# Optimization experiments

Measured on AMD Instinct MI355X. Metric: run time of the kernel, lower is better.

## Reference

```python
import jax, jax.numpy as jnp
import numpy as np

N_T, D_MODEL, RANK, BATCH = 64, 1024, 8, 4096
THRESHOLD = 0.0  # jumprelu threshold (forward default)


def setup_inputs() -> dict:
    key = jax.random.key(0)
    k_x, k_v, k_u, k_e = jax.random.split(key, 4)
    scale = (1.0 / (D_MODEL * RANK)) ** 0.25
    x = jax.random.normal(k_x, (BATCH, D_MODEL), dtype=jnp.float32)
    V = jax.random.normal(k_v, (N_T, RANK, D_MODEL), dtype=jnp.float32) * scale
    U = jax.random.normal(k_u, (N_T, D_MODEL, RANK), dtype=jnp.float32) * scale
    encoder = jax.random.normal(k_e, (N_T, D_MODEL), dtype=jnp.float32)
    encoder = encoder / jnp.linalg.norm(encoder, axis=1, keepdims=True)
    bias = -jnp.ones((N_T,), dtype=jnp.float32)  # init_constant(bias, -1.0)
    return {"x": x, "V": V, "U": U, "encoder": encoder, "bias": bias}


def jumprelu(x, threshold=THRESHOLD):
    # forward: hard threshold x * 1[x > threshold]
    return x * (x > threshold).astype(x.dtype)


def reference(x, V, U, encoder, bias):
    # pre_acts: (batch, n)
    pre_acts = x @ encoder.T - bias
    gate = jumprelu(pre_acts)  # activation_fn='jumprelu', threshold=0.0
    # Vx: (n, batch, rank)
    Vx = jnp.einsum('nrd,bd->nbr', V, x)
    # UVx: (n, batch, d) -- the large intermediate a fused kernel would avoid
    UVx = jnp.einsum('ndr,nbr->nbd', U, Vx)
    # gated sum over transforms: (batch, d)
    output = jnp.einsum('nbd,bn->bd', UVx, gate)
    u_norms = jnp.linalg.norm(U.reshape(U.shape[0], -1), axis=1)
    v_norms = jnp.linalg.norm(V.reshape(V.shape[0], -1), axis=1)
    frobenius_norms = u_norms * v_norms / (D_MODEL * RANK) ** 0.5
    return output, gate, frobenius_norms
```

## Files before the change

### kernel.cpp

```cpp
#include <hip/hip_runtime.h>
#include <math.h>

#define BATCHN 4096
#define DMODEL 1024
#define NT 64
#define RANK 8
#define K2 512

typedef __attribute__((ext_vector_type(8))) short bf16x8;
typedef __attribute__((ext_vector_type(4))) float f32x4;

__device__ __forceinline__ short f2bf_hu(float f) {
    unsigned u = __builtin_bit_cast(unsigned, f);
    return (short)((u + 0x8000u) >> 16);
}

__device__ __forceinline__ short f2bf(float f) {
    unsigned u = __builtin_bit_cast(unsigned, f);
    u += 0x7fffu + ((u >> 16) & 1u);
    return (short)(u >> 16);
}

__device__ __forceinline__ bf16x8 cvt8(const float* __restrict__ p) {
    float4 v0 = *(const float4*)p;
    float4 v1 = *(const float4*)(p + 4);
    bf16x8 o;
    o[0] = f2bf_hu(v0.x); o[1] = f2bf_hu(v0.y); o[2] = f2bf_hu(v0.z); o[3] = f2bf_hu(v0.w);
    o[4] = f2bf_hu(v1.x); o[5] = f2bf_hu(v1.y); o[6] = f2bf_hu(v1.z); o[7] = f2bf_hu(v1.w);
    return o;
}

__global__ __launch_bounds__(256) void gatevx_norms_kernel(
    const float* __restrict__ x, const float* __restrict__ V,
    const float* __restrict__ U, const float* __restrict__ enc,
    const float* __restrict__ bias,
    float* __restrict__ gate, float* __restrict__ fro,
    unsigned short* __restrict__ vx)
{
    __shared__ unsigned short As[64 * 128];
    __shared__ unsigned short Bs[64 * 128];
    __shared__ float red[8];
    const int bid = blockIdx.x, t = threadIdx.x;
    const int wave = t >> 6, lane = t & 63;
    const int wm = wave & 1, wn = wave >> 1;
    const int l15 = lane & 15, lq = lane >> 4;

    if (bid < 576) {
        const int bn = bid % 9, bm = bid / 9;
        const float* Brow = (bn == 0) ? enc : (V + (size_t)(bn - 1) * 64 * DMODEL);
        f32x4 acc[2][2] = {};
        for (int k0 = 0; k0 < DMODEL; k0 += 128) {
            #pragma unroll
            for (int c = 0; c < 4; ++c) {
                const int row = wave * 16 + c * 4 + lq;
                const int g = l15 ^ (row & 15);
                bf16x8 oa = cvt8(x + (size_t)(bm * 64 + row) * DMODEL + k0 + g * 8);
                *(bf16x8*)&As[row * 128 + l15 * 8] = oa;
                bf16x8 ob = cvt8(Brow + (size_t)row * DMODEL + k0 + g * 8);
                *(bf16x8*)&Bs[row * 128 + l15 * 8] = ob;
            }
            __syncthreads();
            #pragma unroll
            for (int s = 0; s < 4; ++s) {
                const int kc = s * 4 + lq;
                bf16x8 af[2], bfr[2];
                #pragma unroll
                for (int i = 0; i < 2; ++i) {
                    const int m = wm * 32 + i * 16 + l15;
                    af[i] = *(const bf16x8*)&As[m * 128 + ((kc ^ (m & 15)) * 8)];
                }
                #pragma unroll
                for (int j = 0; j < 2; ++j) {
                    const int n = wn * 32 + j * 16 + l15;
                    bfr[j] = *(const bf16x8*)&Bs[n * 128 + ((kc ^ (n & 15)) * 8)];
                }
                #pragma unroll
                for (int i = 0; i < 2; ++i)
                    #pragma unroll
                    for (int j = 0; j < 2; ++j)
                        acc[i][j] = __builtin_amdgcn_mfma_f32_16x16x32_bf16(
                            af[i], bfr[j], acc[i][j], 0, 0, 0);
            }
            __syncthreads();
        }
        #pragma unroll
        for (int i = 0; i < 2; ++i) {
            const int rowb = bm * 64 + wm * 32 + i * 16 + lq * 4;
            #pragma unroll
            for (int j = 0; j < 2; ++j) {
                const int col = wn * 32 + j * 16 + l15;
                #pragma unroll
                for (int r = 0; r < 4; ++r) {
                    const int row = rowb + r;
                    const float v = acc[i][j][r];
                    if (bn == 0) {
                        const float p = v - bias[col];
                        gate[(size_t)row * NT + col] = p > 0.f ? p : 0.f;
                    } else {
                        vx[(size_t)row * K2 + (bn - 1) * 64 + col] = (unsigned short)f2bf(v);
                    }
                }
            }
        }
    } else {
        const int n = bid - 576;
        const float* Up = U + (size_t)n * (DMODEL * RANK);
        const float* Vp = V + (size_t)n * (DMODEL * RANK);
        float su = 0.f, sv = 0.f;
        for (int i = t * 4; i < DMODEL * RANK; i += 1024) {
            float4 a = *(const float4*)(Up + i);
            su += a.x * a.x + a.y * a.y + a.z * a.z + a.w * a.w;
            float4 b = *(const float4*)(Vp + i);
            sv += b.x * b.x + b.y * b.y + b.z * b.z + b.w * b.w;
        }
        #pragma unroll
        for (int off = 32; off; off >>= 1) {
            su += __shfl_down(su, off);
            sv += __shfl_down(sv, off);
        }
        if ((t & 63) == 0) { red[wave * 2] = su; red[wave * 2 + 1] = sv; }
        __syncthreads();
        if (t == 0) {
            float tu = red[0] + red[2] + red[4] + red[6];
            float tv = red[1] + red[3] + red[5] + red[7];
            fro[n] = sqrtf(tu) * sqrtf(tv) / sqrtf((float)(DMODEL * RANK));
        }
    }
}

__global__ __launch_bounds__(256) void out_kernel(
    const unsigned short* __restrict__ vx, const float* __restrict__ gate,
    const float* __restrict__ U, float* __restrict__ out)
{
    __shared__ unsigned short As[64 * 128];
    __shared__ unsigned short Bs[16 * 64 * 8];
    const int t = threadIdx.x;
    const int wave = t >> 6, lane = t & 63;
    const int bm = blockIdx.y, bn = blockIdx.x;
    const int wm = wave & 1, wn = wave >> 1;
    const int l15 = lane & 15, lq = lane >> 4;

    f32x4 acc[2][2] = {};

    for (int k0 = 0; k0 < K2; k0 += 128) {
        const int nb = k0 >> 3;
        #pragma unroll
        for (int i = 0; i < 4; ++i) {
            const int row = wave * 16 + i * 4 + lq;
            const int grow = bm * 64 + row;
            const int g = l15 ^ (row & 15);
            bf16x8 v = *(const bf16x8*)(vx + (size_t)grow * K2 + k0 + g * 8);
            const float gs = gate[(size_t)grow * NT + nb + g];
            bf16x8 o;
            #pragma unroll
            for (int e = 0; e < 8; ++e) {
                const float f = __builtin_bit_cast(float,
                    ((unsigned)(unsigned short)v[e]) << 16);
                o[e] = (short)(__builtin_bit_cast(unsigned, f * gs) >> 16);
            }
            *(bf16x8*)&As[row * 128 + l15 * 8] = o;
        }
        #pragma unroll
        for (int c = 0; c < 4; ++c) {
            const int kc = c * 4 + wave;
            bf16x8 o = cvt8(U + (size_t)(nb + kc) * (DMODEL * RANK)
                              + (size_t)(bn * 64 + lane) * RANK);
            *(bf16x8*)&Bs[kc * 512 + lane * 8] = o;
        }
        __syncthreads();
        #pragma unroll
        for (int s = 0; s < 4; ++s) {
            const int kc = s * 4 + lq;
            bf16x8 af[2], bfr[2];
            #pragma unroll
            for (int i = 0; i < 2; ++i) {
                const int m = wm * 32 + i * 16 + l15;
                af[i] = *(const bf16x8*)&As[m * 128 + ((kc ^ (m & 15)) * 8)];
            }
            #pragma unroll
            for (int j = 0; j < 2; ++j) {
                const int n = wn * 32 + j * 16 + l15;
                bfr[j] = *(const bf16x8*)&Bs[kc * 512 + n * 8];
            }
            #pragma unroll
            for (int i = 0; i < 2; ++i)
                #pragma unroll
                for (int j = 0; j < 2; ++j)
                    acc[i][j] = __builtin_amdgcn_mfma_f32_16x16x32_bf16(
                        af[i], bfr[j], acc[i][j], 0, 0, 0);
        }
        __syncthreads();
    }

    #pragma unroll
    for (int i = 0; i < 2; ++i) {
        const int rowb = bm * 64 + wm * 32 + i * 16 + lq * 4;
        #pragma unroll
        for (int j = 0; j < 2; ++j) {
            const int col = bn * 64 + wn * 32 + j * 16 + l15;
            #pragma unroll
            for (int r = 0; r < 4; ++r)
                out[(size_t)(rowb + r) * DMODEL + col] = acc[i][j][r];
        }
    }
}

extern "C" void kernel_launch(void* const* d_in, const int* in_sizes, int n_in,
                              void* d_out, int out_size, void* d_ws, size_t ws_size,
                              hipStream_t stream) {
    const float* x    = (const float*)d_in[0];
    const float* V    = (const float*)d_in[1];
    const float* U    = (const float*)d_in[2];
    const float* enc  = (const float*)d_in[3];
    const float* bias = (const float*)d_in[4];

    float* out  = (float*)d_out;
    float* gate = out + (size_t)BATCHN * DMODEL;
    float* fro  = gate + (size_t)BATCHN * NT;
    unsigned short* vx = (unsigned short*)d_ws;

    gatevx_norms_kernel<<<640, 256, 0, stream>>>(x, V, U, enc, bias, gate, fro, vx);
    out_kernel<<<dim3(16, 64), 256, 0, stream>>>(vx, gate, U, out);
}
```

Measured before the change: 121.0 us.

## Fuse both stages into one persistent kernel with grid barriers and bf16 pre-conversion

Merges the gate/Vx/norms kernel and the output kernel into a single 1024-block kernel separated by software grid barriers. A first phase converts x, encoder/V and U to bf16 in workspace, so the GEMM stages can stage tiles with direct global-to-LDS async loads instead of per-thread fp32 loads and conversions. This aims to cut one launch and reduce load/convert cost in the inner loops. In exchange it adds an extra pass over all inputs, a memset, and spin barriers that need all 1024 blocks co-resident and fall through on timeout, which is a deadlock or correctness risk.

```diff
diff --git a/kernel.cpp b/kernel.cpp
--- a/kernel.cpp
+++ b/kernel.cpp
@@ -9,6 +9,12 @@
 
 typedef __attribute__((ext_vector_type(8))) short bf16x8;
 typedef __attribute__((ext_vector_type(4))) float f32x4;
+
+__device__ __forceinline__ void async16(void* lds, const void* g) {
+    __builtin_amdgcn_global_load_lds(
+        (const __attribute__((address_space(1))) void*)g,
+        (__attribute__((address_space(3))) void*)lds, 16, 0, 0);
+}
 
 __device__ __forceinline__ short f2bf_hu(float f) {
     unsigned u = __builtin_bit_cast(unsigned, f);
@@ -30,12 +36,29 @@
     return o;
 }
 
-__global__ __launch_bounds__(256) void gatevx_norms_kernel(
+__device__ __forceinline__ void grid_barrier(unsigned* c, unsigned n) {
+    __syncthreads();
+    if (threadIdx.x == 0) {
+        __threadfence();
+        atomicAdd(c, 1u);
+        unsigned spins = 0;
+        while (__hip_atomic_load(c, __ATOMIC_RELAXED, __HIP_MEMORY_SCOPE_AGENT) < n) {
+            __builtin_amdgcn_s_sleep(2);
+            if (++spins > 1000000u) break;
+        }
+        __threadfence();
+    }
+    __syncthreads();
+}
+
+__global__ __launch_bounds__(256, 4) void fused_kernel(
     const float* __restrict__ x, const float* __restrict__ V,
     const float* __restrict__ U, const float* __restrict__ enc,
     const float* __restrict__ bias,
-    float* __restrict__ gate, float* __restrict__ fro,
-    unsigned short* __restrict__ vx)
+    float* __restrict__ out, float* __restrict__ gate, float* __restrict__ fro,
+    unsigned short* __restrict__ xb, unsigned short* __restrict__ Wb,
+    unsigned short* __restrict__ Ub, unsigned short* __restrict__ vx,
+    unsigned* __restrict__ counters)
 {
     __shared__ unsigned short As[64 * 128];
     __shared__ unsigned short Bs[64 * 128];
@@ -45,19 +68,41 @@
     const int wm = wave & 1, wn = wave >> 1;
     const int l15 = lane & 15, lq = lane >> 4;
 
+    {
+        const int tid = bid * 256 + t;
+        for (int c = tid; c < 663552; c += 262144) {
+            const float* src;
+            unsigned short* dst;
+            if (c < 524288) {
+                src = x + (size_t)c * 8; dst = xb + (size_t)c * 8;
+            } else if (c < 598016) {
+                const int e = (c - 524288) * 8;
+                const int row = e >> 10, col = e & 1023;
+                src = (row < 64) ? (enc + (size_t)row * 1024 + col)
+                                 : (V + (size_t)(row - 64) * 1024 + col);
+                dst = Wb + e;
+            } else {
+                const int e = (c - 598016) * 8;
+                src = U + e; dst = Ub + e;
+            }
+            *(bf16x8*)dst = cvt8(src);
+        }
+    }
+    grid_barrier(&counters[0], (unsigned)gridDim.x);
+
     if (bid < 576) {
         const int bn = bid % 9, bm = bid / 9;
-        const float* Brow = (bn == 0) ? enc : (V + (size_t)(bn - 1) * 64 * DMODEL);
         f32x4 acc[2][2] = {};
+        const size_t Abase = (size_t)bm * 64 * DMODEL;
+        const size_t Bbase = (size_t)bn * 64 * DMODEL;
         for (int k0 = 0; k0 < DMODEL; k0 += 128) {
             #pragma unroll
             for (int c = 0; c < 4; ++c) {
-                const int row = wave * 16 + c * 4 + lq;
+                const int r0 = wave * 16 + c * 4;
+                const int row = r0 + lq;
                 const int g = l15 ^ (row & 15);
-                bf16x8 oa = cvt8(x + (size_t)(bm * 64 + row) * DMODEL + k0 + g * 8);
-                *(bf16x8*)&As[row * 128 + l15 * 8] = oa;
-                bf16x8 ob = cvt8(Brow + (size_t)row * DMODEL + k0 + g * 8);
-                *(bf16x8*)&Bs[row * 128 + l15 * 8] = ob;
+                async16(&As[r0 * 128], xb + Abase + (size_t)row * DMODEL + k0 + g * 8);
+                async16(&Bs[r0 * 128], Wb + Bbase + (size_t)row * DMODEL + k0 + g * 8);
             }
             __syncthreads();
             #pragma unroll
@@ -102,7 +147,7 @@
                 }
             }
         }
-    } else {
+    } else if (bid < 640) {
         const int n = bid - 576;
         const float* Up = U + (size_t)n * (DMODEL * RANK);
         const float* Vp = V + (size_t)n * (DMODEL * RANK);
@@ -126,81 +171,70 @@
             fro[n] = sqrtf(tu) * sqrtf(tv) / sqrtf((float)(DMODEL * RANK));
         }
     }
-}
-
-__global__ __launch_bounds__(256) void out_kernel(
-    const unsigned short* __restrict__ vx, const float* __restrict__ gate,
-    const float* __restrict__ U, float* __restrict__ out)
-{
-    __shared__ unsigned short As[64 * 128];
-    __shared__ unsigned short Bs[16 * 64 * 8];
-    const int t = threadIdx.x;
-    const int wave = t >> 6, lane = t & 63;
-    const int bm = blockIdx.y, bn = blockIdx.x;
-    const int wm = wave & 1, wn = wave >> 1;
-    const int l15 = lane & 15, lq = lane >> 4;
-
-    f32x4 acc[2][2] = {};
-
-    for (int k0 = 0; k0 < K2; k0 += 128) {
-        const int nb = k0 >> 3;
+    grid_barrier(&counters[1], (unsigned)gridDim.x);
+
+    {
+        const int bn = bid & 15, bm = bid >> 4;
+        f32x4 acc[2][2] = {};
+        for (int k0 = 0; k0 < K2; k0 += 128) {
+            const int nb = k0 >> 3;
+            #pragma unroll
+            for (int i = 0; i < 4; ++i) {
+                const int row = wave * 16 + i * 4 + lq;
+                const int grow = bm * 64 + row;
+                const int g = l15 ^ (row & 15);
+                bf16x8 v = *(const bf16x8*)(vx + (size_t)grow * K2 + k0 + g * 8);
+                const float gs = gate[(size_t)grow * NT + nb + g];
+                bf16x8 o;
+                #pragma unroll
+                for (int e = 0; e < 8; ++e) {
+                    const float f = __builtin_bit_cast(float,
+                        ((unsigned)(unsigned short)v[e]) << 16);
+                    o[e] = (short)(__builtin_bit_cast(unsigned, f * gs) >> 16);
+                }
+                *(bf16x8*)&As[row * 128 + l15 * 8] = o;
+            }
+            #pragma unroll
+            for (int c = 0; c < 4; ++c) {
+                const int kc = c * 4 + wave;
+                async16(&Bs[kc * 512],
+                        Ub + (size_t)(nb + kc) * (DMODEL * RANK)
+                           + (size_t)(bn * 64 + lane) * RANK);
+            }
+            __syncthreads();
+            #pragma unroll
+            for (int s = 0; s < 4; ++s) {
+                const int kc = s * 4 + lq;
+                bf16x8 af[2], bfr[2];
+                #pragma unroll
+                for (int i = 0; i < 2; ++i) {
+                    const int m = wm * 32 + i * 16 + l15;
+                    af[i] = *(const bf16x8*)&As[m * 128 + ((kc ^ (m & 15)) * 8)];
+                }
+                #pragma unroll
+                for (int j = 0; j < 2; ++j) {
+                    const int n = wn * 32 + j * 16 + l15;
+                    bfr[j] = *(const bf16x8*)&Bs[kc * 512 + n * 8];
+                }
+                #pragma unroll
+                for (int i = 0; i < 2; ++i)
+                    #pragma unroll
+                    for (int j = 0; j < 2; ++j)
+                        acc[i][j] = __builtin_amdgcn_mfma_f32_16x16x32_bf16(
+                            af[i], bfr[j], acc[i][j], 0, 0, 0);
+            }
+            __syncthreads();
+        }
         #pragma unroll
-        for (int i = 0; i < 4; ++i) {
-            const int row = wave * 16 + i * 4 + lq;
-            const int grow = bm * 64 + row;
-            const int g = l15 ^ (row & 15);
-            bf16x8 v = *(const bf16x8*)(vx + (size_t)grow * K2 + k0 + g * 8);
-            const float gs = gate[(size_t)grow * NT + nb + g];
-            bf16x8 o;
-            #pragma unroll
-            for (int e = 0; e < 8; ++e) {
-                const float f = __builtin_bit_cast(float,
-                    ((unsigned)(unsigned short)v[e]) << 16);
-                o[e] = (short)(__builtin_bit_cast(unsigned, f * gs) >> 16);
-            }
-            *(bf16x8*)&As[row * 128 + l15 * 8] = o;
-        }
-        #pragma unroll
-        for (int c = 0; c < 4; ++c) {
-            const int kc = c * 4 + wave;
-            bf16x8 o = cvt8(U + (size_t)(nb + kc) * (DMODEL * RANK)
-                              + (size_t)(bn * 64 + lane) * RANK);
-            *(bf16x8*)&Bs[kc * 512 + lane * 8] = o;
-        }
-        __syncthreads();
-        #pragma unroll
-        for (int s = 0; s < 4; ++s) {
-            const int kc = s * 4 + lq;
-            bf16x8 af[2], bfr[2];
-            #pragma unroll
-            for (int i = 0; i < 2; ++i) {
-                const int m = wm * 32 + i * 16 + l15;
-                af[i] = *(const bf16x8*)&As[m * 128 + ((kc ^ (m & 15)) * 8)];
-            }
+        for (int i = 0; i < 2; ++i) {
+            const int rowb = bm * 64 + wm * 32 + i * 16 + lq * 4;
             #pragma unroll
             for (int j = 0; j < 2; ++j) {
-                const int n = wn * 32 + j * 16 + l15;
-                bfr[j] = *(const bf16x8*)&Bs[kc * 512 + n * 8];
-            }
-            #pragma unroll
-            for (int i = 0; i < 2; ++i)
-                #pragma unroll
-                for (int j = 0; j < 2; ++j)
-                    acc[i][j] = __builtin_amdgcn_mfma_f32_16x16x32_bf16(
-                        af[i], bfr[j], acc[i][j], 0, 0, 0);
-        }
-        __syncthreads();
-    }
-
-    #pragma unroll
-    for (int i = 0; i < 2; ++i) {
-        const int rowb = bm * 64 + wm * 32 + i * 16 + lq * 4;
-        #pragma unroll
-        for (int j = 0; j < 2; ++j) {
-            const int col = bn * 64 + wn * 32 + j * 16 + l15;
-            #pragma unroll
-            for (int r = 0; r < 4; ++r)
-                out[(size_t)(rowb + r) * DMODEL + col] = acc[i][j][r];
+                const int col = bn * 64 + wn * 32 + j * 16 + l15;
+                #pragma unroll
+                for (int r = 0; r < 4; ++r)
+                    out[(size_t)(rowb + r) * DMODEL + col] = acc[i][j][r];
+            }
         }
     }
 }
@@ -217,8 +251,15 @@
     float* out  = (float*)d_out;
     float* gate = out + (size_t)BATCHN * DMODEL;
     float* fro  = gate + (size_t)BATCHN * NT;
-    unsigned short* vx = (unsigned short*)d_ws;
-
-    gatevx_norms_kernel<<<640, 256, 0, stream>>>(x, V, U, enc, bias, gate, fro, vx);
-    out_kernel<<<dim3(16, 64), 256, 0, stream>>>(vx, gate, U, out);
-}
+
+    char* ws = (char*)d_ws;
+    unsigned short* xb = (unsigned short*)ws;
+    unsigned short* Wb = (unsigned short*)(ws + 8388608);
+    unsigned short* Ub = (unsigned short*)(ws + 9568256);
+    unsigned short* vx = (unsigned short*)(ws + 10616832);
+    unsigned* counters = (unsigned*)(ws + 14811136);
+
+    hipMemsetAsync(counters, 0, 2 * sizeof(unsigned), stream);
+    fused_kernel<<<1024, 256, 0, stream>>>(x, V, U, enc, bias, out, gate, fro,
+                                           xb, Wb, Ub, vx, counters);
+}
```

Result: slower. 337.3 us (+178.7%).
